# Optimization experiments

Hardware: AMD Instinct MI355X
Metric: run time of the kernel (lower is better)

Reference implementation:

```python
import jax, jax.numpy as jnp
import numpy as np

COMMITMENT_COST = 0.25
NUM_EMBEDDINGS = 512
EMBEDDING_DIM = 64


def setup_inputs() -> dict:
    key = jax.random.key(0)
    k1, k2 = jax.random.split(key)
    B, T = 64, 1024
    inputs = jax.random.normal(k1, (B, T, EMBEDDING_DIM), dtype=jnp.float32)
    # matches nn.Embedding init uniform_(-1/K, 1/K)
    embedding = jax.random.uniform(
        k2, (NUM_EMBEDDINGS, EMBEDDING_DIM), dtype=jnp.float32,
        minval=-1.0 / NUM_EMBEDDINGS, maxval=1.0 / NUM_EMBEDDINGS)
    return {"inputs": inputs, "embedding": embedding}


def reference(inputs, embedding):
    B = inputs.shape[0]
    K, D = embedding.shape
    flat = inputs.reshape(-1, D)  # [N, D]
    # squared-euclidean distances [N, K] (same expansion as torch source)
    distances = (
        jnp.sum(flat * flat, axis=1, keepdims=True)
        + jnp.sum(embedding * embedding, axis=1)
        - 2.0 * flat @ embedding.T
    )
    idx = jnp.argmin(distances, axis=1)  # [N]
    # one-hot @ embedding  ==  gather
    quantized = embedding[idx].reshape(inputs.shape)

    e_latent_loss = jnp.mean((jax.lax.stop_gradient(quantized) - inputs) ** 2)
    q_latent_loss = jnp.mean((quantized - jax.lax.stop_gradient(inputs)) ** 2)
    loss = q_latent_loss + COMMITMENT_COST * e_latent_loss

    # straight-through estimator
    quantized_st = inputs + jax.lax.stop_gradient(quantized - inputs)

    # avg_probs = mean of one-hot encodings == histogram of indices / N
    counts = jax.ops.segment_sum(
        jnp.ones(flat.shape[0], dtype=jnp.float32), idx, num_segments=K)
    avg_probs = counts / flat.shape[0]
    perplexity = jnp.exp(-jnp.sum(avg_probs * jnp.log(avg_probs + 1e-10)))

    indices_for_transformer = idx.reshape(B, -1)
    return loss, quantized_st, perplexity, indices_for_transformer
```

## Files before the change

### kernel.cpp

```cpp
#include <hip/hip_runtime.h>
#include <math.h>

#define D 64
#define K 512
#define BLOCK 256
#define KSLICE 64
#define NSLICES 8
#define NPART 32


__device__ __forceinline__ float np_sumsq64(const float* v) {
#pragma clang fp contract(off)
    float r[8];
#pragma unroll
    for (int m = 0; m < 8; ++m) r[m] = v[m] * v[m];
#pragma unroll
    for (int i = 8; i < 64; i += 8) {
#pragma unroll
        for (int m = 0; m < 8; ++m) r[m] = r[m] + v[i + m] * v[i + m];
    }
    return ((r[0] + r[1]) + (r[2] + r[3])) + ((r[4] + r[5]) + (r[6] + r[7]));
}

__global__ __launch_bounds__(BLOCK, 4) void vq_scan(
    const float* __restrict__ x, const float* __restrict__ emb,
    float* __restrict__ stash, int N)
{
    __shared__ float se_s[KSLICE];

    const int tid = threadIdx.x;
    const int kbase = blockIdx.y * KSLICE;

    if (tid < KSLICE) {
        float er[D];
        const float4* e4 = (const float4*)(emb + (size_t)(kbase + tid) * D);
#pragma unroll
        for (int j = 0; j < D / 4; ++j) {
            float4 v = e4[j];
            er[4 * j + 0] = v.x; er[4 * j + 1] = v.y;
            er[4 * j + 2] = v.z; er[4 * j + 3] = v.w;
        }
        se_s[tid] = np_sumsq64(er);
    }
    __syncthreads();

    const int row = blockIdx.x * BLOCK + tid;
    if (row >= N) return;

    float xr[D];
    {
        const float4* xp = (const float4*)(x + (size_t)row * D);
#pragma unroll
        for (int j = 0; j < D / 4; ++j) {
            float4 v = xp[j];
            xr[4 * j + 0] = v.x; xr[4 * j + 1] = v.y;
            xr[4 * j + 2] = v.z; xr[4 * j + 3] = v.w;
        }
    }
    const float sx = np_sumsq64(xr);

    const float* ebase = emb + (size_t)kbase * D;
    float bestd = INFINITY;
    int bi = 0;
    for (int k = 0; k < KSLICE; k += 4) {
        float a0 = 0.f, a1 = 0.f, a2 = 0.f, a3 = 0.f;
        const float4* e0 = (const float4*)(ebase + (size_t)(k + 0) * D);
        const float4* e1 = (const float4*)(ebase + (size_t)(k + 1) * D);
        const float4* e2 = (const float4*)(ebase + (size_t)(k + 2) * D);
        const float4* e3 = (const float4*)(ebase + (size_t)(k + 3) * D);
#pragma unroll
        for (int j = 0; j < D / 4; ++j) {
            float4 ea = e0[j];
            float4 eb = e1[j];
            float4 ec = e2[j];
            float4 ed = e3[j];
            a0 = fmaf(xr[4 * j + 0], ea.x, a0);
            a1 = fmaf(xr[4 * j + 0], eb.x, a1);
            a2 = fmaf(xr[4 * j + 0], ec.x, a2);
            a3 = fmaf(xr[4 * j + 0], ed.x, a3);
            a0 = fmaf(xr[4 * j + 1], ea.y, a0);
            a1 = fmaf(xr[4 * j + 1], eb.y, a1);
            a2 = fmaf(xr[4 * j + 1], ec.y, a2);
            a3 = fmaf(xr[4 * j + 1], ed.y, a3);
            a0 = fmaf(xr[4 * j + 2], ea.z, a0);
            a1 = fmaf(xr[4 * j + 2], eb.z, a1);
            a2 = fmaf(xr[4 * j + 2], ec.z, a2);
            a3 = fmaf(xr[4 * j + 2], ed.z, a3);
            a0 = fmaf(xr[4 * j + 3], ea.w, a0);
            a1 = fmaf(xr[4 * j + 3], eb.w, a1);
            a2 = fmaf(xr[4 * j + 3], ec.w, a2);
            a3 = fmaf(xr[4 * j + 3], ed.w, a3);
        }
        const float4 se4 = *(const float4*)&se_s[k];
        float d0 = (sx + se4.x) - 2.0f * a0;
        float d1 = (sx + se4.y) - 2.0f * a1;
        float d2 = (sx + se4.z) - 2.0f * a2;
        float d3 = (sx + se4.w) - 2.0f * a3;
        if (d0 < bestd) { bestd = d0; bi = k; }
        if (d1 < bestd) { bestd = d1; bi = k + 1; }
        if (d2 < bestd) { bestd = d2; bi = k + 2; }
        if (d3 < bestd) { bestd = d3; bi = k + 3; }
    }

    float2 p; p.x = bestd; p.y = (float)(kbase + bi);
    *(float2*)(stash + (size_t)row * D + 2 * blockIdx.y) = p;
}

__global__ __launch_bounds__(BLOCK) void vq_merge(
    const float* __restrict__ x, const float* __restrict__ emb,
    float* __restrict__ q_out, float* __restrict__ idx_out,
    float* __restrict__ block_sums, int* __restrict__ part_hist, int N)
{
    __shared__ int hist[K];
    __shared__ float red[BLOCK / 64];
    const int tid = threadIdx.x;
    for (int k = tid; k < K; k += BLOCK) hist[k] = 0;
    __syncthreads();

    const int row = blockIdx.x * BLOCK + tid;
    float s = 0.f;
    if (row < N) {
        float bestd = INFINITY;
        int bi = 0;
#pragma unroll
        for (int sl = 0; sl < NSLICES; ++sl) {
            float2 p = *(const float2*)(q_out + (size_t)row * D + 2 * sl);
            if (p.x < bestd) { bestd = p.x; bi = (int)p.y; }
        }
        atomicAdd(&hist[bi], 1);

        const float4* xp = (const float4*)(x + (size_t)row * D);
        const float4* ep = (const float4*)(emb + (size_t)bi * D);
        float4* qp = (float4*)(q_out + (size_t)row * D);
#pragma unroll
        for (int j = 0; j < D / 4; ++j) {
            float4 xv = xp[j];
            float4 e  = ep[j];
            float dx0 = e.x - xv.x, dx1 = e.y - xv.y;
            float dx2 = e.z - xv.z, dx3 = e.w - xv.w;
            s = fmaf(dx0, dx0, s);
            s = fmaf(dx1, dx1, s);
            s = fmaf(dx2, dx2, s);
            s = fmaf(dx3, dx3, s);
            float4 qs;
            qs.x = xv.x + dx0; qs.y = xv.y + dx1;
            qs.z = xv.z + dx2; qs.w = xv.w + dx3;
            qp[j] = qs;
        }
        idx_out[row] = (float)bi;
    }

    for (int off = 32; off; off >>= 1) s += __shfl_down(s, off, 64);
    if ((tid & 63) == 0) red[tid >> 6] = s;
    __syncthreads();
    if (tid == 0) {
        float t = 0.f;
#pragma unroll
        for (int w = 0; w < BLOCK / 64; ++w) t += red[w];
        block_sums[blockIdx.x] = t;
    }
    const int part = (int)(blockIdx.x & (NPART - 1));
    for (int k = tid; k < K; k += BLOCK) {
        int h = hist[k];
        if (h) atomicAdd(&part_hist[part * K + k], h);
    }
}

__global__ __launch_bounds__(512) void vq_finalize(
    const float* __restrict__ block_sums, int nblocks,
    const int* __restrict__ part_hist, float* __restrict__ out_loss,
    float* __restrict__ out_perp, float inv_nelem, float inv_rows)
{
    const int tid = threadIdx.x;
    double ls = 0.0;
    for (int i = tid; i < nblocks; i += 512) ls += (double)block_sums[i];
    int c = 0;
#pragma unroll
    for (int pp = 0; pp < NPART; ++pp) c += part_hist[pp * K + tid];
    double ps = 0.0;
    {
        float p = (float)c * inv_rows;
        ps = (double)(p * logf(p + 1e-10f));
    }
    for (int off = 32; off; off >>= 1) {
        ls += __shfl_down(ls, off, 64);
        ps += __shfl_down(ps, off, 64);
    }
    __shared__ double l8[8], p8[8];
    if ((tid & 63) == 0) { l8[tid >> 6] = ls; p8[tid >> 6] = ps; }
    __syncthreads();
    if (tid == 0) {
        double L = 0.0, P = 0.0;
#pragma unroll
        for (int w = 0; w < 8; ++w) { L += l8[w]; P += p8[w]; }
        *out_loss = 1.25f * (float)(L * (double)inv_nelem);
        *out_perp = expf((float)(-P));
    }
}

extern "C" void kernel_launch(void* const* d_in, const int* in_sizes, int n_in,
                              void* d_out, int out_size, void* d_ws, size_t ws_size,
                              hipStream_t stream) {
    const float* x   = (const float*)d_in[0];
    const float* emb = (const float*)d_in[1];
    const int N = in_sizes[0] / D;
    const int nblocks = (N + BLOCK - 1) / BLOCK;

    float* out      = (float*)d_out;
    float* loss_out = out;
    float* q_out    = out + 1;
    float* perp_out = out + 1 + (size_t)N * D;
    float* idx_out  = perp_out + 1;

    float* block_sums = (float*)d_ws;
    int*   part_hist  = (int*)((char*)d_ws + (((size_t)nblocks * 4 + 255) & ~(size_t)255));

    hipMemsetAsync(part_hist, 0, NPART * K * sizeof(int), stream);
    dim3 sgrid(nblocks, NSLICES);
    vq_scan<<<sgrid, BLOCK, 0, stream>>>(x, emb, q_out, N);
    vq_merge<<<nblocks, BLOCK, 0, stream>>>(x, emb, q_out, idx_out,
                                            block_sums, part_hist, N);
    vq_finalize<<<1, 512, 0, stream>>>(block_sums, nblocks, part_hist,
                                       loss_out, perp_out,
                                       1.0f / (float)((size_t)N * D),
                                       1.0f / (float)N);
}
```

Measured before the change: 167.1 us.

## Fuse scan and merge into one shared-memory tiled distance kernel

```diff
diff --git a/kernel.cpp b/kernel.cpp
--- a/kernel.cpp
+++ b/kernel.cpp
@@ -4,8 +4,9 @@
 #define D 64
 #define K 512
 #define BLOCK 256
-#define KSLICE 64
-#define NSLICES 8
+#define ROWS 128
+#define KT 128
+#define NKT (K / KT)
 #define NPART 32
 
 
@@ -22,120 +23,143 @@
     return ((r[0] + r[1]) + (r[2] + r[3])) + ((r[4] + r[5]) + (r[6] + r[7]));
 }
 
-__global__ __launch_bounds__(BLOCK, 4) void vq_scan(
-    const float* __restrict__ x, const float* __restrict__ emb,
-    float* __restrict__ stash, int N)
-{
-    __shared__ float se_s[KSLICE];
-
-    const int tid = threadIdx.x;
-    const int kbase = blockIdx.y * KSLICE;
-
-    if (tid < KSLICE) {
-        float er[D];
-        const float4* e4 = (const float4*)(emb + (size_t)(kbase + tid) * D);
-#pragma unroll
-        for (int j = 0; j < D / 4; ++j) {
-            float4 v = e4[j];
-            er[4 * j + 0] = v.x; er[4 * j + 1] = v.y;
-            er[4 * j + 2] = v.z; er[4 * j + 3] = v.w;
-        }
-        se_s[tid] = np_sumsq64(er);
-    }
-    __syncthreads();
-
-    const int row = blockIdx.x * BLOCK + tid;
-    if (row >= N) return;
-
-    float xr[D];
-    {
-        const float4* xp = (const float4*)(x + (size_t)row * D);
-#pragma unroll
-        for (int j = 0; j < D / 4; ++j) {
-            float4 v = xp[j];
-            xr[4 * j + 0] = v.x; xr[4 * j + 1] = v.y;
-            xr[4 * j + 2] = v.z; xr[4 * j + 3] = v.w;
-        }
-    }
-    const float sx = np_sumsq64(xr);
-
-    const float* ebase = emb + (size_t)kbase * D;
-    float bestd = INFINITY;
-    int bi = 0;
-    for (int k = 0; k < KSLICE; k += 4) {
-        float a0 = 0.f, a1 = 0.f, a2 = 0.f, a3 = 0.f;
-        const float4* e0 = (const float4*)(ebase + (size_t)(k + 0) * D);
-        const float4* e1 = (const float4*)(ebase + (size_t)(k + 1) * D);
-        const float4* e2 = (const float4*)(ebase + (size_t)(k + 2) * D);
-        const float4* e3 = (const float4*)(ebase + (size_t)(k + 3) * D);
-#pragma unroll
-        for (int j = 0; j < D / 4; ++j) {
-            float4 ea = e0[j];
-            float4 eb = e1[j];
-            float4 ec = e2[j];
-            float4 ed = e3[j];
-            a0 = fmaf(xr[4 * j + 0], ea.x, a0);
-            a1 = fmaf(xr[4 * j + 0], eb.x, a1);
-            a2 = fmaf(xr[4 * j + 0], ec.x, a2);
-            a3 = fmaf(xr[4 * j + 0], ed.x, a3);
-            a0 = fmaf(xr[4 * j + 1], ea.y, a0);
-            a1 = fmaf(xr[4 * j + 1], eb.y, a1);
-            a2 = fmaf(xr[4 * j + 1], ec.y, a2);
-            a3 = fmaf(xr[4 * j + 1], ed.y, a3);
-            a0 = fmaf(xr[4 * j + 2], ea.z, a0);
-            a1 = fmaf(xr[4 * j + 2], eb.z, a1);
-            a2 = fmaf(xr[4 * j + 2], ec.z, a2);
-            a3 = fmaf(xr[4 * j + 2], ed.z, a3);
-            a0 = fmaf(xr[4 * j + 3], ea.w, a0);
-            a1 = fmaf(xr[4 * j + 3], eb.w, a1);
-            a2 = fmaf(xr[4 * j + 3], ec.w, a2);
-            a3 = fmaf(xr[4 * j + 3], ed.w, a3);
-        }
-        const float4 se4 = *(const float4*)&se_s[k];
-        float d0 = (sx + se4.x) - 2.0f * a0;
-        float d1 = (sx + se4.y) - 2.0f * a1;
-        float d2 = (sx + se4.z) - 2.0f * a2;
-        float d3 = (sx + se4.w) - 2.0f * a3;
-        if (d0 < bestd) { bestd = d0; bi = k; }
-        if (d1 < bestd) { bestd = d1; bi = k + 1; }
-        if (d2 < bestd) { bestd = d2; bi = k + 2; }
-        if (d3 < bestd) { bestd = d3; bi = k + 3; }
-    }
-
-    float2 p; p.x = bestd; p.y = (float)(kbase + bi);
-    *(float2*)(stash + (size_t)row * D + 2 * blockIdx.y) = p;
-}
-
-__global__ __launch_bounds__(BLOCK) void vq_merge(
+__global__ __launch_bounds__(BLOCK, 2) void vq_fused(
     const float* __restrict__ x, const float* __restrict__ emb,
     float* __restrict__ q_out, float* __restrict__ idx_out,
     float* __restrict__ block_sums, int* __restrict__ part_hist, int N)
 {
+    __shared__ float4 xs4[ROWS * 16];
+    __shared__ float4 es4[KT * 16];
+    __shared__ float sx_s[ROWS];
+    __shared__ float se_s[KT];
     __shared__ int hist[K];
     __shared__ float red[BLOCK / 64];
+
     const int tid = threadIdx.x;
-    for (int k = tid; k < K; k += BLOCK) hist[k] = 0;
-    __syncthreads();
-
-    const int row = blockIdx.x * BLOCK + tid;
+    const int rg = tid & 15;
+    const int cg = tid >> 4;
+    const int rowbase = blockIdx.x * ROWS;
+
+    for (int k2 = tid; k2 < K; k2 += BLOCK) hist[k2] = 0;
+
+    const float4* xsrc = (const float4*)(x + (size_t)rowbase * D);
+#pragma unroll
+    for (int i = 0; i < (ROWS * 16) / BLOCK; ++i) {
+        int f = tid + i * BLOCK;
+        int row = f >> 4, jc = f & 15;
+        xs4[row * 16 + (jc ^ ((row >> 3) & 7))] = xsrc[f];
+    }
+    __syncthreads();
+
+    if (tid < ROWS) {
+        float xr[D];
+        const int sw = (tid >> 3) & 7;
+#pragma unroll
+        for (int jc = 0; jc < 16; ++jc) {
+            float4 v = xs4[tid * 16 + (jc ^ sw)];
+            xr[4 * jc + 0] = v.x; xr[4 * jc + 1] = v.y;
+            xr[4 * jc + 2] = v.z; xr[4 * jc + 3] = v.w;
+        }
+        sx_s[tid] = np_sumsq64(xr);
+    }
+
+    float bd[8], bkf[8];
+#pragma unroll
+    for (int r = 0; r < 8; ++r) { bd[r] = INFINITY; bkf[r] = 0.f; }
+
+    const int xbase = rg * 8, ebase = cg * 8;
+    const int swx0 = rg & 7, swe0 = cg & 7;
+
+    for (int kt = 0; kt < NKT; ++kt) {
+        const float4* esrc = (const float4*)(emb + (size_t)kt * KT * D);
+#pragma unroll
+        for (int i = 0; i < (KT * 16) / BLOCK; ++i) {
+            int f = tid + i * BLOCK;
+            int row = f >> 4, jc = f & 15;
+            es4[row * 16 + (jc ^ ((row >> 3) & 7))] = esrc[f];
+        }
+        __syncthreads();
+
+        if (tid < KT) {
+            float er[D];
+            const int sw = (tid >> 3) & 7;
+#pragma unroll
+            for (int jc = 0; jc < 16; ++jc) {
+                float4 v = es4[tid * 16 + (jc ^ sw)];
+                er[4 * jc + 0] = v.x; er[4 * jc + 1] = v.y;
+                er[4 * jc + 2] = v.z; er[4 * jc + 3] = v.w;
+            }
+            se_s[tid] = np_sumsq64(er);
+        }
+
+        float acc[8][8];
+#pragma unroll
+        for (int r = 0; r < 8; ++r)
+#pragma unroll
+            for (int c = 0; c < 8; ++c) acc[r][c] = 0.f;
+
+#pragma unroll 2
+        for (int jc = 0; jc < 16; ++jc) {
+            float4 xa[8], eb[8];
+#pragma unroll
+            for (int r = 0; r < 8; ++r)
+                xa[r] = xs4[(xbase + r) * 16 + (jc ^ swx0)];
+#pragma unroll
+            for (int c = 0; c < 8; ++c)
+                eb[c] = es4[(ebase + c) * 16 + (jc ^ swe0)];
+#pragma unroll
+            for (int r = 0; r < 8; ++r)
+#pragma unroll
+                for (int c = 0; c < 8; ++c) {
+                    acc[r][c] = fmaf(xa[r].x, eb[c].x, acc[r][c]);
+                    acc[r][c] = fmaf(xa[r].y, eb[c].y, acc[r][c]);
+                    acc[r][c] = fmaf(xa[r].z, eb[c].z, acc[r][c]);
+                    acc[r][c] = fmaf(xa[r].w, eb[c].w, acc[r][c]);
+                }
+        }
+        __syncthreads();
+
+        const int kglob = kt * KT + ebase;
+        float sev[8];
+#pragma unroll
+        for (int c = 0; c < 8; ++c) sev[c] = se_s[ebase + c];
+#pragma unroll
+        for (int r = 0; r < 8; ++r) {
+            float sxv = sx_s[xbase + r];
+#pragma unroll
+            for (int c = 0; c < 8; ++c) {
+                float dcur = (sxv + sev[c]) - 2.0f * acc[r][c];
+                if (dcur < bd[r]) { bd[r] = dcur; bkf[r] = (float)(kglob + c); }
+            }
+        }
+    }
+
+    __syncthreads();
+    float2* bests = (float2*)es4;
+#pragma unroll
+    for (int r = 0; r < 8; ++r)
+        bests[(xbase + r) * 16 + cg] = make_float2(bd[r], bkf[r]);
+    __syncthreads();
+
     float s = 0.f;
-    if (row < N) {
-        float bestd = INFINITY;
-        int bi = 0;
-#pragma unroll
-        for (int sl = 0; sl < NSLICES; ++sl) {
-            float2 p = *(const float2*)(q_out + (size_t)row * D + 2 * sl);
-            if (p.x < bestd) { bestd = p.x; bi = (int)p.y; }
-        }
+    if (tid < ROWS) {
+        float bdd = INFINITY, bjf = 1e30f;
+#pragma unroll
+        for (int g = 0; g < 16; ++g) {
+            float2 p = bests[tid * 16 + g];
+            if (p.x < bdd || (p.x == bdd && p.y < bjf)) { bdd = p.x; bjf = p.y; }
+        }
+        const int bi = (int)bjf;
         atomicAdd(&hist[bi], 1);
 
-        const float4* xp = (const float4*)(x + (size_t)row * D);
+        const int rowg = rowbase + tid;
         const float4* ep = (const float4*)(emb + (size_t)bi * D);
-        float4* qp = (float4*)(q_out + (size_t)row * D);
-#pragma unroll
-        for (int j = 0; j < D / 4; ++j) {
-            float4 xv = xp[j];
-            float4 e  = ep[j];
+        float4* qp = (float4*)(q_out + (size_t)rowg * D);
+        const int sw = (tid >> 3) & 7;
+#pragma unroll
+        for (int jc = 0; jc < 16; ++jc) {
+            float4 xv = xs4[tid * 16 + (jc ^ sw)];
+            float4 e  = ep[jc];
             float dx0 = e.x - xv.x, dx1 = e.y - xv.y;
             float dx2 = e.z - xv.z, dx3 = e.w - xv.w;
             s = fmaf(dx0, dx0, s);
@@ -145,9 +169,9 @@
             float4 qs;
             qs.x = xv.x + dx0; qs.y = xv.y + dx1;
             qs.z = xv.z + dx2; qs.w = xv.w + dx3;
-            qp[j] = qs;
-        }
-        idx_out[row] = (float)bi;
+            qp[jc] = qs;
+        }
+        idx_out[rowg] = (float)bi;
     }
 
     for (int off = 32; off; off >>= 1) s += __shfl_down(s, off, 64);
@@ -160,9 +184,9 @@
         block_sums[blockIdx.x] = t;
     }
     const int part = (int)(blockIdx.x & (NPART - 1));
-    for (int k = tid; k < K; k += BLOCK) {
-        int h = hist[k];
-        if (h) atomicAdd(&part_hist[part * K + k], h);
+    for (int k2 = tid; k2 < K; k2 += BLOCK) {
+        int h = hist[k2];
+        if (h) atomicAdd(&part_hist[part * K + k2], h);
     }
 }
 
@@ -204,7 +228,7 @@
     const float* x   = (const float*)d_in[0];
     const float* emb = (const float*)d_in[1];
     const int N = in_sizes[0] / D;
-    const int nblocks = (N + BLOCK - 1) / BLOCK;
+    const int nblocks = N / ROWS;
 
     float* out      = (float*)d_out;
     float* loss_out = out;
@@ -216,9 +240,7 @@
     int*   part_hist  = (int*)((char*)d_ws + (((size_t)nblocks * 4 + 255) & ~(size_t)255));
 
     hipMemsetAsync(part_hist, 0, NPART * K * sizeof(int), stream);
-    dim3 sgrid(nblocks, NSLICES);
-    vq_scan<<<sgrid, BLOCK, 0, stream>>>(x, emb, q_out, N);
-    vq_merge<<<nblocks, BLOCK, 0, stream>>>(x, emb, q_out, idx_out,
+    vq_fused<<<nblocks, BLOCK, 0, stream>>>(x, emb, q_out, idx_out,
                                             block_sums, part_hist, N);
     vq_finalize<<<1, 512, 0, stream>>>(block_sums, nblocks, part_hist,
                                        loss_out, perp_out,
```

After: 139.8 us. 1.2x faster.

## Fuse scan and merge into one kernel with per-wave codebook slices

Applied to the files above, without the earlier changes.

```diff
diff --git a/kernel.cpp b/kernel.cpp
--- a/kernel.cpp
+++ b/kernel.cpp
@@ -4,8 +4,9 @@
 #define D 64
 #define K 512
 #define BLOCK 256
-#define KSLICE 64
-#define NSLICES 8
+#define ROWS 64
+#define KW 128
+#define CH 8
 #define NPART 32
 
 
@@ -22,36 +23,43 @@
     return ((r[0] + r[1]) + (r[2] + r[3])) + ((r[4] + r[5]) + (r[6] + r[7]));
 }
 
-__global__ __launch_bounds__(BLOCK, 4) void vq_scan(
+__global__ __launch_bounds__(64) void vq_se(
+    const float* __restrict__ emb, float* __restrict__ se_ws)
+{
+    const int k = blockIdx.x * 64 + threadIdx.x;
+    float er[D];
+    const float4* e4 = (const float4*)(emb + (size_t)k * D);
+#pragma unroll
+    for (int j = 0; j < 16; ++j) {
+        float4 v = e4[j];
+        er[4 * j + 0] = v.x; er[4 * j + 1] = v.y;
+        er[4 * j + 2] = v.z; er[4 * j + 3] = v.w;
+    }
+    se_ws[k] = np_sumsq64(er);
+}
+
+__global__ __launch_bounds__(BLOCK, 4) void vq_main(
     const float* __restrict__ x, const float* __restrict__ emb,
-    float* __restrict__ stash, int N)
+    const float* __restrict__ se_ws,
+    float* __restrict__ q_out, float* __restrict__ idx_out,
+    float* __restrict__ block_sums, int* __restrict__ part_hist, int N)
 {
-    __shared__ float se_s[KSLICE];
+    __shared__ float2 bests[4 * ROWS];
+    __shared__ int hist[K];
 
     const int tid = threadIdx.x;
-    const int kbase = blockIdx.y * KSLICE;
-
-    if (tid < KSLICE) {
-        float er[D];
-        const float4* e4 = (const float4*)(emb + (size_t)(kbase + tid) * D);
-#pragma unroll
-        for (int j = 0; j < D / 4; ++j) {
-            float4 v = e4[j];
-            er[4 * j + 0] = v.x; er[4 * j + 1] = v.y;
-            er[4 * j + 2] = v.z; er[4 * j + 3] = v.w;
-        }
-        se_s[tid] = np_sumsq64(er);
-    }
-    __syncthreads();
-
-    const int row = blockIdx.x * BLOCK + tid;
-    if (row >= N) return;
+    const int lane = tid & 63;
+    const int wv = __builtin_amdgcn_readfirstlane(tid >> 6);
+    const int rowbase = blockIdx.x * ROWS;
+    const int row = rowbase + lane;
+
+    for (int k2 = tid; k2 < K; k2 += BLOCK) hist[k2] = 0;
 
     float xr[D];
     {
         const float4* xp = (const float4*)(x + (size_t)row * D);
 #pragma unroll
-        for (int j = 0; j < D / 4; ++j) {
+        for (int j = 0; j < 16; ++j) {
             float4 v = xp[j];
             xr[4 * j + 0] = v.x; xr[4 * j + 1] = v.y;
             xr[4 * j + 2] = v.z; xr[4 * j + 3] = v.w;
@@ -59,110 +67,78 @@
     }
     const float sx = np_sumsq64(xr);
 
-    const float* ebase = emb + (size_t)kbase * D;
-    float bestd = INFINITY;
-    int bi = 0;
-    for (int k = 0; k < KSLICE; k += 4) {
-        float a0 = 0.f, a1 = 0.f, a2 = 0.f, a3 = 0.f;
-        const float4* e0 = (const float4*)(ebase + (size_t)(k + 0) * D);
-        const float4* e1 = (const float4*)(ebase + (size_t)(k + 1) * D);
-        const float4* e2 = (const float4*)(ebase + (size_t)(k + 2) * D);
-        const float4* e3 = (const float4*)(ebase + (size_t)(k + 3) * D);
-#pragma unroll
-        for (int j = 0; j < D / 4; ++j) {
-            float4 ea = e0[j];
-            float4 eb = e1[j];
-            float4 ec = e2[j];
-            float4 ed = e3[j];
-            a0 = fmaf(xr[4 * j + 0], ea.x, a0);
-            a1 = fmaf(xr[4 * j + 0], eb.x, a1);
-            a2 = fmaf(xr[4 * j + 0], ec.x, a2);
-            a3 = fmaf(xr[4 * j + 0], ed.x, a3);
-            a0 = fmaf(xr[4 * j + 1], ea.y, a0);
-            a1 = fmaf(xr[4 * j + 1], eb.y, a1);
-            a2 = fmaf(xr[4 * j + 1], ec.y, a2);
-            a3 = fmaf(xr[4 * j + 1], ed.y, a3);
-            a0 = fmaf(xr[4 * j + 2], ea.z, a0);
-            a1 = fmaf(xr[4 * j + 2], eb.z, a1);
-            a2 = fmaf(xr[4 * j + 2], ec.z, a2);
-            a3 = fmaf(xr[4 * j + 2], ed.z, a3);
-            a0 = fmaf(xr[4 * j + 3], ea.w, a0);
-            a1 = fmaf(xr[4 * j + 3], eb.w, a1);
-            a2 = fmaf(xr[4 * j + 3], ec.w, a2);
-            a3 = fmaf(xr[4 * j + 3], ed.w, a3);
-        }
-        const float4 se4 = *(const float4*)&se_s[k];
-        float d0 = (sx + se4.x) - 2.0f * a0;
-        float d1 = (sx + se4.y) - 2.0f * a1;
-        float d2 = (sx + se4.z) - 2.0f * a2;
-        float d3 = (sx + se4.w) - 2.0f * a3;
-        if (d0 < bestd) { bestd = d0; bi = k; }
-        if (d1 < bestd) { bestd = d1; bi = k + 1; }
-        if (d2 < bestd) { bestd = d2; bi = k + 2; }
-        if (d3 < bestd) { bestd = d3; bi = k + 3; }
-    }
-
-    float2 p; p.x = bestd; p.y = (float)(kbase + bi);
-    *(float2*)(stash + (size_t)row * D + 2 * blockIdx.y) = p;
-}
-
-__global__ __launch_bounds__(BLOCK) void vq_merge(
-    const float* __restrict__ x, const float* __restrict__ emb,
-    float* __restrict__ q_out, float* __restrict__ idx_out,
-    float* __restrict__ block_sums, int* __restrict__ part_hist, int N)
-{
-    __shared__ int hist[K];
-    __shared__ float red[BLOCK / 64];
-    const int tid = threadIdx.x;
-    for (int k = tid; k < K; k += BLOCK) hist[k] = 0;
+    float bd = INFINITY, bk = 0.f;
+    const int wk = wv * KW;
+    for (int ch = 0; ch < KW / CH; ++ch) {
+        const int kb = wk + ch * CH;
+        const float* ew = emb + (size_t)kb * D;
+        const float* sep = se_ws + kb;
+        float a[CH];
+#pragma unroll
+        for (int c = 0; c < CH; ++c) a[c] = 0.f;
+#pragma unroll
+        for (int jc = 0; jc < 16; ++jc) {
+            const float xv0 = xr[4 * jc + 0], xv1 = xr[4 * jc + 1];
+            const float xv2 = xr[4 * jc + 2], xv3 = xr[4 * jc + 3];
+#pragma unroll
+            for (int c = 0; c < CH; ++c) {
+                const float4 ev = *(const float4*)(ew + c * D + 4 * jc);
+                a[c] = fmaf(xv0, ev.x, a[c]);
+                a[c] = fmaf(xv1, ev.y, a[c]);
+                a[c] = fmaf(xv2, ev.z, a[c]);
+                a[c] = fmaf(xv3, ev.w, a[c]);
+            }
+        }
+#pragma unroll
+        for (int c = 0; c < CH; ++c) {
+            float dcur = (sx + sep[c]) - 2.0f * a[c];
+            if (dcur < bd) { bd = dcur; bk = (float)(kb + c); }
+        }
+    }
+
+    bests[wv * ROWS + lane] = make_float2(bd, bk);
     __syncthreads();
 
-    const int row = blockIdx.x * BLOCK + tid;
-    float s = 0.f;
-    if (row < N) {
-        float bestd = INFINITY;
-        int bi = 0;
-#pragma unroll
-        for (int sl = 0; sl < NSLICES; ++sl) {
-            float2 p = *(const float2*)(q_out + (size_t)row * D + 2 * sl);
-            if (p.x < bestd) { bestd = p.x; bi = (int)p.y; }
-        }
+    if (tid < ROWS) {
+        float bdd = INFINITY, bjf = 1e30f;
+#pragma unroll
+        for (int w = 0; w < 4; ++w) {
+            float2 p = bests[w * ROWS + tid];
+            if (p.x < bdd || (p.x == bdd && p.y < bjf)) { bdd = p.x; bjf = p.y; }
+        }
+        const int bi = (int)bjf;
         atomicAdd(&hist[bi], 1);
 
-        const float4* xp = (const float4*)(x + (size_t)row * D);
         const float4* ep = (const float4*)(emb + (size_t)bi * D);
         float4* qp = (float4*)(q_out + (size_t)row * D);
-#pragma unroll
-        for (int j = 0; j < D / 4; ++j) {
-            float4 xv = xp[j];
-            float4 e  = ep[j];
-            float dx0 = e.x - xv.x, dx1 = e.y - xv.y;
-            float dx2 = e.z - xv.z, dx3 = e.w - xv.w;
+        float s = 0.f;
+#pragma unroll
+        for (int jc = 0; jc < 16; ++jc) {
+            float4 e = ep[jc];
+            float x0 = xr[4 * jc + 0], x1 = xr[4 * jc + 1];
+            float x2 = xr[4 * jc + 2], x3 = xr[4 * jc + 3];
+            float dx0 = e.x - x0, dx1 = e.y - x1;
+            float dx2 = e.z - x2, dx3 = e.w - x3;
             s = fmaf(dx0, dx0, s);
             s = fmaf(dx1, dx1, s);
             s = fmaf(dx2, dx2, s);
             s = fmaf(dx3, dx3, s);
             float4 qs;
-            qs.x = xv.x + dx0; qs.y = xv.y + dx1;
-            qs.z = xv.z + dx2; qs.w = xv.w + dx3;
-            qp[j] = qs;
+            qs.x = x0 + dx0; qs.y = x1 + dx1;
+            qs.z = x2 + dx2; qs.w = x3 + dx3;
+            qp[jc] = qs;
         }
         idx_out[row] = (float)bi;
-    }
-
-    for (int off = 32; off; off >>= 1) s += __shfl_down(s, off, 64);
-    if ((tid & 63) == 0) red[tid >> 6] = s;
+
+        for (int off = 32; off; off >>= 1) s += __shfl_down(s, off, 64);
+        if (tid == 0) block_sums[blockIdx.x] = s;
+    }
+
     __syncthreads();
-    if (tid == 0) {
-        float t = 0.f;
-#pragma unroll
-        for (int w = 0; w < BLOCK / 64; ++w) t += red[w];
-        block_sums[blockIdx.x] = t;
-    }
     const int part = (int)(blockIdx.x & (NPART - 1));
-    for (int k = tid; k < K; k += BLOCK) {
-        int h = hist[k];
-        if (h) atomicAdd(&part_hist[part * K + k], h);
+    for (int k2 = tid; k2 < K; k2 += BLOCK) {
+        int h = hist[k2];
+        if (h) atomicAdd(&part_hist[part * K + k2], h);
     }
 }
 
@@ -204,7 +180,7 @@
     const float* x   = (const float*)d_in[0];
     const float* emb = (const float*)d_in[1];
     const int N = in_sizes[0] / D;
-    const int nblocks = (N + BLOCK - 1) / BLOCK;
+    const int nblocks = N / ROWS;
 
     float* out      = (float*)d_out;
     float* loss_out = out;
@@ -213,13 +189,14 @@
     float* idx_out  = perp_out + 1;
 
     float* block_sums = (float*)d_ws;
-    int*   part_hist  = (int*)((char*)d_ws + (((size_t)nblocks * 4 + 255) & ~(size_t)255));
+    char*  base       = (char*)d_ws;
+    int*   part_hist  = (int*)(base + (((size_t)nblocks * 4 + 255) & ~(size_t)255));
+    float* se_ws      = (float*)((char*)part_hist + (size_t)NPART * K * sizeof(int));
 
     hipMemsetAsync(part_hist, 0, NPART * K * sizeof(int), stream);
-    dim3 sgrid(nblocks, NSLICES);
-    vq_scan<<<sgrid, BLOCK, 0, stream>>>(x, emb, q_out, N);
-    vq_merge<<<nblocks, BLOCK, 0, stream>>>(x, emb, q_out, idx_out,
-                                            block_sums, part_hist, N);
+    vq_se<<<dim3(K / 64), 64, 0, stream>>>(emb, se_ws);
+    vq_main<<<nblocks, BLOCK, 0, stream>>>(x, emb, se_ws, q_out, idx_out,
+                                           block_sums, part_hist, N);
     vq_finalize<<<1, 512, 0, stream>>>(block_sums, nblocks, part_hist,
                                        loss_out, perp_out,
                                        1.0f / (float)((size_t)N * D),
```

After: 237.6 us. 1.42x slower.
